# Kernel optimization log

Hardware: AMD Instinct MI355X
Metric: run time of the kernel (lower is better)

Reference implementation:

```python
import jax, jax.numpy as jnp
import numpy as np

EMBED_DIM = 512
NUM_HEADS = 8
HEAD_DIM = EMBED_DIM // NUM_HEADS
LN_EPS = 1e-5


def setup_inputs() -> dict:
    key = jax.random.key(0)
    ks = jax.random.split(key, 7)
    B, S, E = 2, 4096, EMBED_DIM
    s = 1.0 / np.sqrt(E)
    return {
        "x": jax.random.normal(ks[0], (B, S, E), dtype=jnp.float32),
        "qkv_w": jax.random.normal(ks[1], (E, 3 * E), dtype=jnp.float32) * s,
        "qkv_b": jax.random.normal(ks[2], (3 * E,), dtype=jnp.float32) * 0.01,
        "out_w": jax.random.normal(ks[3], (E, E), dtype=jnp.float32) * s,
        "out_b": jax.random.normal(ks[4], (E,), dtype=jnp.float32) * 0.01,
        "ln_g": jnp.ones((E,), dtype=jnp.float32),
        "ln_b": jnp.zeros((E,), dtype=jnp.float32),
    }


def reference(x, qkv_w, qkv_b, out_w, out_b, ln_g, ln_b):
    B, S, E = x.shape
    H, D = NUM_HEADS, HEAD_DIM
    scale = D ** -0.5
    qkv = x @ qkv_w + qkv_b                     # (B, S, 3E)
    qkv = qkv.reshape(B, S, 3, H, D)
    q, k, v = qkv[:, :, 0], qkv[:, :, 1], qkv[:, :, 2]  # (B, S, H, D)
    scores = jnp.einsum("bshd,bthd->bhst", q, k) * scale  # (B, H, S, S)
    probs = jax.nn.softmax(scores, axis=-1)
    ctx = jnp.einsum("bhst,bthd->bshd", probs, v).reshape(B, S, E)
    out = ctx @ out_w + out_b + x               # residual
    mu = out.mean(-1, keepdims=True)
    var = out.var(-1, keepdims=True)
    return (out - mu) * jax.lax.rsqrt(var + LN_EPS) * ln_g + ln_b
```

## Files before the change

kernel.cpp:

```cpp
#include <hip/hip_runtime.h>
#include <stdint.h>

typedef __bf16 bf16x8 __attribute__((ext_vector_type(8)));
typedef float f32x4 __attribute__((ext_vector_type(4)));
typedef float f32x16 __attribute__((ext_vector_type(16)));
typedef float float4v __attribute__((ext_vector_type(4)));
typedef unsigned short u16x4 __attribute__((ext_vector_type(4)));
typedef unsigned short u16x8 __attribute__((ext_vector_type(8)));
typedef unsigned int u32x4v __attribute__((ext_vector_type(4)));

#define DEVI __device__ __forceinline__

static constexpr int Bv = 2, Sv = 4096, Ev = 512, Hv = 8, Dv = 64;
static constexpr int Mv = Bv * Sv;
static constexpr int N3v = 3 * Ev;
static constexpr float QSCALE = 0.125f * 1.4426950408889634f;
static constexpr float C0 = -8.0f;

#if __has_builtin(__builtin_amdgcn_exp2f)
#define EXP2F(x) __builtin_amdgcn_exp2f(x)
#else
#define EXP2F(x) exp2f(x)
#endif

DEVI unsigned short f2bf(float f) {
    unsigned int u = __builtin_bit_cast(unsigned int, f);
    u += 0x7fffu + ((u >> 16) & 1u);
    return (unsigned short)(u >> 16);
}

DEVI float b2f(unsigned short u) {
    return __builtin_bit_cast(float, (unsigned int)u << 16);
}

DEVI unsigned int cvtpk(float lo, float hi) {
    unsigned int r;
    asm("v_cvt_pk_bf16_f32 %0, %1, %2" : "=v"(r) : "v"(lo), "v"(hi));
    return r;
}

DEVI void gload16(const void* src, void* lds) {
    __builtin_amdgcn_global_load_lds(
        (const __attribute__((address_space(1))) unsigned int*)src,
        (__attribute__((address_space(3))) unsigned int*)lds,
        16, 0, 0);
}

__global__ __launch_bounds__(256) void k_prep(const float* __restrict__ x,
                                              unsigned short* __restrict__ xb,
                                              const float* __restrict__ qkv_w,
                                              unsigned short* __restrict__ wqkvT,
                                              const float* __restrict__ out_w,
                                              unsigned short* __restrict__ owT) {
    __shared__ float lds[32][36];
    int blk = blockIdx.x;
    int t = threadIdx.x;
    if (blk < 2048) {
        int n4 = Mv * Ev / 4;
        int i = blk * 256 + t;
        int stride = 2048 * 256;
        for (; i < n4; i += stride) {
            float4v v = ((const float4v*)x)[i];
            u16x4 o;
            o[0] = f2bf(v[0]); o[1] = f2bf(v[1]); o[2] = f2bf(v[2]); o[3] = f2bf(v[3]);
            ((u16x4*)xb)[i] = o;
        }
        return;
    }
    const float* in;
    unsigned short* out;
    int K = 512, N, tile;
    if (blk < 2816) { in = qkv_w; out = wqkvT; N = 1536; tile = blk - 2048; }
    else            { in = out_w; out = owT;   N = 512;  tile = blk - 2816; }
    int tilesN = N >> 5;
    int tn = tile % tilesN, tk = tile / tilesN;
    int k0 = tk << 5, n0 = tn << 5;
    int r = t >> 3, c4 = (t & 7) << 2;
    float4v v = *(const float4v*)(in + (size_t)(k0 + r) * N + n0 + c4);
    *(float4v*)&lds[r][c4] = v;
    __syncthreads();
    int nn = t >> 3, kc = (t & 7) << 2;
    u16x4 o;
#pragma unroll
    for (int j = 0; j < 4; ++j) o[j] = f2bf(lds[kc + j][nn]);
    *(u16x4*)(out + (size_t)(n0 + nn) * K + k0 + kc) = o;
}

template <int EPI>
__global__ __launch_bounds__(256) void k_gemm(
    const unsigned short* __restrict__ A, const unsigned short* __restrict__ Bt,
    int M, int N, int K, const float* __restrict__ bias,
    unsigned short* __restrict__ Qb, unsigned short* __restrict__ Kb,
    unsigned short* __restrict__ Vtb,
    const float* __restrict__ xres, unsigned short* __restrict__ outb) {
    __shared__ char smem[32768];
    char* As = smem;
    char* Bs = smem + 16384;
    int nbt = N >> 7;
    int mb = blockIdx.x / nbt, nbi = blockIdx.x % nbt;
    int m0 = mb << 7, n0 = nbi << 7;
    int tid = threadIdx.x, lane = tid & 63, wave = tid >> 6;
    int wr = wave >> 1, wc = wave & 1;

    f32x4 acc[4][4];
    f32x4 zero = {0.f, 0.f, 0.f, 0.f};
#pragma unroll
    for (int a = 0; a < 4; ++a)
#pragma unroll
        for (int b = 0; b < 4; ++b) acc[a][b] = zero;

    for (int kt = 0; kt < K; kt += 64) {
        __syncthreads();
#pragma unroll
        for (int j = 0; j < 4; ++j) {
            int la = (((wave << 2) + j) << 10) + lane * 16;
            int r = la >> 7, cb = la & 127;
            int cbs = cb ^ ((r & 7) << 4);
            gload16((const char*)(A + (size_t)(m0 + r) * K + kt) + cbs,
                    As + (((wave << 2) + j) << 10));
            gload16((const char*)(Bt + (size_t)(n0 + r) * K + kt) + cbs,
                    Bs + (((wave << 2) + j) << 10));
        }
        asm volatile("s_waitcnt vmcnt(0)" ::: "memory");
        __syncthreads();

        bf16x8 af[4][2], bfr[4][2];
#pragma unroll
        for (int rf = 0; rf < 4; ++rf)
#pragma unroll
            for (int c = 0; c < 2; ++c) {
                int row = (wr << 6) + (rf << 4) + (lane & 15);
                int col = (c << 6) + ((lane >> 4) << 4);
                af[rf][c] = *(const bf16x8*)(As + row * 128 + (col ^ ((row & 7) << 4)));
                int rowb = (wc << 6) + (rf << 4) + (lane & 15);
                bfr[rf][c] = *(const bf16x8*)(Bs + rowb * 128 + (col ^ ((rowb & 7) << 4)));
            }
#pragma unroll
        for (int rf = 0; rf < 4; ++rf)
#pragma unroll
            for (int nf = 0; nf < 4; ++nf)
#pragma unroll
                for (int c = 0; c < 2; ++c)
                    acc[rf][nf] = __builtin_amdgcn_mfma_f32_16x16x32_bf16(
                        af[rf][c], bfr[nf][c], acc[rf][nf], 0, 0, 0);
    }

#pragma unroll
    for (int rf = 0; rf < 4; ++rf)
#pragma unroll
        for (int nf = 0; nf < 4; ++nf) {
            int row0 = m0 + (wr << 6) + (rf << 4) + ((lane >> 4) << 2);
            int col = n0 + (wc << 6) + (nf << 4) + (lane & 15);
            float bv = bias[col];
            if (EPI == 0) {
                int reg = col >> 9, hd = col & 511;
                int h = hd >> 6, d = hd & 63;
                int b = row0 >> 12, s0 = row0 & 4095;
                if (reg == 2) {
                    u16x4 o4;
#pragma unroll
                    for (int i = 0; i < 4; ++i) o4[i] = f2bf(acc[rf][nf][i] + bv);
                    *(u16x4*)(Vtb + ((size_t)((b << 3) + h) * 64 + d) * 4096 + s0) = o4;
                } else {
#pragma unroll
                    for (int i = 0; i < 4; ++i) {
                        float v = acc[rf][nf][i] + bv;
                        size_t idx = ((size_t)((b << 3) + h) * Sv + s0 + i) * Dv + d;
                        if (reg == 0) Qb[idx] = f2bf(v * QSCALE);
                        else          Kb[idx] = f2bf(v);
                    }
                }
            } else {
#pragma unroll
                for (int i = 0; i < 4; ++i) {
                    int row = row0 + i;
                    float v = acc[rf][nf][i] + bv + xres[(size_t)row * N + col];
                    outb[(size_t)row * N + col] = f2bf(v);
                }
            }
        }
}

__global__ __launch_bounds__(256, 2) void k_attn(const unsigned short* __restrict__ Qb,
                                                 const unsigned short* __restrict__ Kb,
                                                 const unsigned short* __restrict__ Vtb,
                                                 unsigned short* __restrict__ po,
                                                 float* __restrict__ pl) {
    __shared__ char smem[24576];
    int bid = blockIdx.x;
    int wg = ((bid & 7) << 6) + (bid >> 3);
    int half = wg & 1, qblk = (wg >> 1) & 15, bh = wg >> 5;
    int tid = threadIdx.x, lane = tid & 63, wave = tid >> 6;
    int l31 = lane & 31, hh = lane >> 5;
    int qbase = (qblk << 8) + (wave << 6);
    int kvbase = half << 11;
    const int NCH = 64;

    const char* Kbase = (const char*)(Kb + (size_t)bh * Sv * Dv + (size_t)kvbase * Dv);
    const char* Vtbase = (const char*)(Vtb + (size_t)bh * Dv * Sv + kvbase);

    bf16x8 qf[2][4];
#pragma unroll
    for (int qs = 0; qs < 2; ++qs)
#pragma unroll
        for (int tp = 0; tp < 4; ++tp)
            qf[qs][tp] = *(const bf16x8*)(Qb + ((size_t)bh * Sv + qbase + (qs << 5) + l31) * Dv +
                                          (tp << 4) + (hh << 3));

    const char* src0;
    const char* src1;
    size_t st0, st1;
    int d0, d1;
    {
        int j0 = wave << 1, j1 = j0 + 1;
        if (j0 < 4) {
            int lo0 = (j0 << 10) + lane * 16, r0 = lo0 >> 7, cb0 = lo0 & 127;
            src0 = Kbase + (size_t)r0 * 128 + (cb0 ^ ((r0 & 7) << 4));
            st0 = 4096; d0 = j0 << 10;
            int lo1 = (j1 << 10) + lane * 16, r1 = lo1 >> 7, cb1 = lo1 & 127;
            src1 = Kbase + (size_t)r1 * 128 + (cb1 ^ ((r1 & 7) << 4));
            st1 = 4096; d1 = j1 << 10;
        } else {
            int lo0 = ((j0 - 4) << 10) + lane * 16, r0 = lo0 >> 6, cb0 = lo0 & 63;
            src0 = Vtbase + (size_t)r0 * 8192 + (cb0 ^ ((r0 & 6) << 3));
            st0 = 64; d0 = 4096 + ((j0 - 4) << 10);
            int lo1 = ((j1 - 4) << 10) + lane * 16, r1 = lo1 >> 6, cb1 = lo1 & 63;
            src1 = Vtbase + (size_t)r1 * 8192 + (cb1 ^ ((r1 & 6) << 3));
            st1 = 64; d1 = 4096 + ((j1 - 4) << 10);
        }
    }

    int koff[4], voff[4];
#pragma unroll
    for (int tp = 0; tp < 4; ++tp)
        koff[tp] = l31 * 128 + (((tp << 5) + (hh << 4)) ^ ((l31 & 7) << 4));
#pragma unroll
    for (int tl = 0; tl < 2; ++tl)
#pragma unroll
        for (int dt = 0; dt < 2; ++dt) {
            int row = (dt << 5) + l31;
            int col = (tl << 5) + (hh << 4);
            voff[tl * 2 + dt] = row * 64 + (col ^ ((row & 6) << 3));
        }

    f32x16 o[2][2];
#pragma unroll
    for (int qs = 0; qs < 2; ++qs)
#pragma unroll
        for (int dt = 0; dt < 2; ++dt)
#pragma unroll
            for (int r = 0; r < 16; ++r) o[qs][dt][r] = 0.f;
    float lsum[2] = {0.f, 0.f};

    gload16(src0, smem + d0);
    gload16(src1, smem + d1);
    gload16(src0 + st0, smem + 8192 + d0);
    gload16(src1 + st1, smem + 8192 + d1);

#define COMPUTE_CHUNK(KSP, VSP)                                                          \
    {                                                                                    \
        bf16x8 kf[4], vf[4];                                                             \
        _Pragma("unroll") for (int tp = 0; tp < 4; ++tp)                                 \
            kf[tp] = *(const bf16x8*)((KSP) + koff[tp]);                                 \
        _Pragma("unroll") for (int i = 0; i < 4; ++i)                                    \
            vf[i] = *(const bf16x8*)((VSP) + voff[i]);                                   \
        _Pragma("unroll") for (int qs = 0; qs < 2; ++qs) {                               \
            f32x16 sc;                                                                   \
            _Pragma("unroll") for (int r = 0; r < 16; ++r) sc[r] = C0;                   \
            __builtin_amdgcn_s_setprio(1);                                               \
            _Pragma("unroll") for (int tp = 0; tp < 4; ++tp)                             \
                sc = __builtin_amdgcn_mfma_f32_32x32x16_bf16(kf[tp], qf[qs][tp], sc, 0, 0, 0); \
            __builtin_amdgcn_s_setprio(0);                                               \
            _Pragma("unroll") for (int r = 0; r < 16; ++r) sc[r] = EXP2F(sc[r]);         \
            float s0 = (sc[0] + sc[1]) + (sc[2] + sc[3]);                                \
            float s1 = (sc[4] + sc[5]) + (sc[6] + sc[7]);                                \
            float s2 = (sc[8] + sc[9]) + (sc[10] + sc[11]);                              \
            float s3 = (sc[12] + sc[13]) + (sc[14] + sc[15]);                            \
            lsum[qs] += (s0 + s1) + (s2 + s3);                                           \
            unsigned int W[8];                                                           \
            _Pragma("unroll") for (int i = 0; i < 8; ++i)                                \
                W[i] = cvtpk(sc[2 * i], sc[2 * i + 1]);                                  \
            _Pragma("unroll") for (int tl = 0; tl < 2; ++tl) {                           \
                unsigned int a1 = W[4 * tl], b1 = W[4 * tl + 2];                         \
                unsigned int a2 = W[4 * tl + 1], b2 = W[4 * tl + 3];                     \
                asm volatile("v_permlane32_swap_b32 %0, %1" : "+v"(a1), "+v"(b1));       \
                asm volatile("v_permlane32_swap_b32 %0, %1" : "+v"(a2), "+v"(b2));       \
                u32x4v uu;                                                               \
                uu[0] = a1; uu[1] = a2; uu[2] = b1; uu[3] = b2;                          \
                bf16x8 pf = __builtin_bit_cast(bf16x8, uu);                              \
                __builtin_amdgcn_s_setprio(1);                                           \
                _Pragma("unroll") for (int dt = 0; dt < 2; ++dt)                         \
                    o[qs][dt] = __builtin_amdgcn_mfma_f32_32x32x16_bf16(                 \
                        vf[tl * 2 + dt], pf, o[qs][dt], 0, 0, 0);                        \
                __builtin_amdgcn_s_setprio(0);                                           \
            }                                                                            \
        }                                                                                \
    }

    int cur = 0;
    for (int kt = 0; kt < NCH - 1; ++kt) {
        asm volatile("s_waitcnt vmcnt(2)\n\ts_barrier" ::: "memory");
        if (kt + 2 < NCH) {
            int tb = cur + 2; if (tb >= 3) tb -= 3;
            gload16(src0 + (size_t)(kt + 2) * st0, smem + tb * 8192 + d0);
            gload16(src1 + (size_t)(kt + 2) * st1, smem + tb * 8192 + d1);
        }
        char* cbuf = smem + cur * 8192;
        COMPUTE_CHUNK(cbuf, cbuf + 4096);
        cur = (cur + 1 == 3) ? 0 : cur + 1;
    }
    asm volatile("s_waitcnt vmcnt(0)\n\ts_barrier" ::: "memory");
    {
        char* cbuf = smem + cur * 8192;
        COMPUTE_CHUNK(cbuf, cbuf + 4096);
    }
#undef COMPUTE_CHUNK

#pragma unroll
    for (int qs = 0; qs < 2; ++qs) {
        float ls = lsum[qs] + __shfl_xor(lsum[qs], 32, 64);
        int qrow = qbase + (qs << 5) + l31;
        if (!hh) pl[((size_t)half * 16 + bh) * Sv + qrow] = ls;
        size_t obase = (((size_t)half * 16 + bh) * Sv + qrow) * 64;
#pragma unroll
        for (int dt = 0; dt < 2; ++dt)
#pragma unroll
            for (int rp = 0; rp < 8; ++rp) {
                int r = rp << 1;
                int d = (dt << 5) + (r & 3) + ((r >> 2) << 3) + (hh << 2);
                unsigned int w = cvtpk(o[qs][dt][r], o[qs][dt][r + 1]);
                *(unsigned int*)(po + obase + d) = w;
            }
    }
}

__global__ __launch_bounds__(256) void k_merge(const unsigned short* __restrict__ po,
                                               const float* __restrict__ pl,
                                               unsigned short* __restrict__ ctx) {
    int t = blockIdx.x * 256 + threadIdx.x;
    int d8 = t & 7, s = (t >> 3) & 4095, bh = t >> 15;
    int b = bh >> 3, h = bh & 7;
    size_t r0 = ((size_t)bh * 4096 + s) * 64 + (d8 << 3);
    size_t r1 = r0 + (size_t)16 * 4096 * 64;
    u16x8 pa = *(const u16x8*)(po + r0);
    u16x8 pb = *(const u16x8*)(po + r1);
    float inv = 1.f / (pl[(size_t)bh * 4096 + s] + pl[(size_t)16 * 4096 + bh * 4096 + s]);
    u32x4v w;
#pragma unroll
    for (int j = 0; j < 4; ++j) {
        float lo = (b2f(pa[2 * j]) + b2f(pb[2 * j])) * inv;
        float hi = (b2f(pa[2 * j + 1]) + b2f(pb[2 * j + 1])) * inv;
        w[j] = cvtpk(lo, hi);
    }
    *(u32x4v*)(ctx + ((size_t)b * 4096 + s) * 512 + (h << 6) + (d8 << 3)) = w;
}

__global__ __launch_bounds__(256) void k_ln(const unsigned short* __restrict__ in,
                                            const float* __restrict__ g,
                                            const float* __restrict__ bta,
                                            float* __restrict__ out) {
    int wave = threadIdx.x >> 6, lane = threadIdx.x & 63;
    size_t row = (size_t)blockIdx.x * 4 + wave;
    u16x8 raw = *(const u16x8*)(in + row * 512 + lane * 8);
    float v[8];
    float s = 0.f, q = 0.f;
#pragma unroll
    for (int j = 0; j < 8; ++j) {
        v[j] = b2f(raw[j]);
        s += v[j];
        q += v[j] * v[j];
    }
#pragma unroll
    for (int off = 1; off < 64; off <<= 1) {
        s += __shfl_xor(s, off, 64);
        q += __shfl_xor(q, off, 64);
    }
    float mu = s * (1.f / 512.f);
    float var = q * (1.f / 512.f) - mu * mu;
    float rs = rsqrtf(var + 1e-5f);
    int c = lane * 8;
    float4v o0, o1;
#pragma unroll
    for (int j = 0; j < 4; ++j) {
        o0[j] = (v[j] - mu) * rs * g[c + j] + bta[c + j];
        o1[j] = (v[4 + j] - mu) * rs * g[c + 4 + j] + bta[c + 4 + j];
    }
    *(float4v*)(out + row * 512 + c) = o0;
    *(float4v*)(out + row * 512 + c + 4) = o1;
}

extern "C" void kernel_launch(void* const* d_in, const int* in_sizes, int n_in,
                              void* d_out, int out_size, void* d_ws, size_t ws_size,
                              hipStream_t stream) {
    const float* x     = (const float*)d_in[0];
    const float* qkv_w = (const float*)d_in[1];
    const float* qkv_b = (const float*)d_in[2];
    const float* out_w = (const float*)d_in[3];
    const float* out_b = (const float*)d_in[4];
    const float* ln_g  = (const float*)d_in[5];
    const float* ln_b  = (const float*)d_in[6];
    float* out = (float*)d_out;
    char* ws = (char*)d_ws;

    unsigned short* owT   = (unsigned short*)(ws);
    unsigned short* wqkvT = (unsigned short*)(ws + 524288);
    unsigned short* Qb    = (unsigned short*)(ws + 2097152);
    unsigned short* Kb    = (unsigned short*)(ws + 10485760);
    unsigned short* Vtb   = (unsigned short*)(ws + 18874368);
    unsigned short* xb    = (unsigned short*)(ws + 27262976);
    unsigned short* po    = (unsigned short*)(ws + 27262976);
    float* pl             = (float*)(ws + 60817408);
    unsigned short* ctxb  = (unsigned short*)(ws + 2097152);
    unsigned short* tmpb  = (unsigned short*)(ws + 10485760);

    k_prep<<<3072, 256, 0, stream>>>(x, xb, qkv_w, wqkvT, out_w, owT);
    k_gemm<0><<<(Mv / 128) * (N3v / 128), 256, 0, stream>>>(
        xb, wqkvT, Mv, N3v, Ev, qkv_b, Qb, Kb, Vtb, nullptr, nullptr);
    k_attn<<<512, 256, 0, stream>>>(Qb, Kb, Vtb, po, pl);
    k_merge<<<2048, 256, 0, stream>>>(po, pl, ctxb);
    k_gemm<1><<<(Mv / 128) * (Ev / 128), 256, 0, stream>>>(
        ctxb, owT, Mv, Ev, Ev, out_b, nullptr, nullptr, nullptr, x, tmpb);
    k_ln<<<Mv / 4, 256, 0, stream>>>(tmpb, ln_g, ln_b, out);
}
```

Baseline: 143.0 us.

## Fuse split-KV merge into attention kernel via last-arriver atomic flag

Removes the separate merge kernel launch. Each attention block now fences its partial output and increments a per-(head, query-block) counter, and the second of the two KV-half blocks to arrive combines both partials and writes the normalized context. This saves a kernel launch and a pass over the partials, and the merge reads data that was just written and may still be in cache. In exchange it adds a memset, atomics and threadfences, and the merge work now runs on only half the attention blocks with a per-thread strided access pattern.

Result: slower. 250.4 us (+75.1%).

```diff
diff --git a/kernel.cpp b/kernel.cpp
--- a/kernel.cpp
+++ b/kernel.cpp
@@ -185,8 +185,11 @@
                                                  const unsigned short* __restrict__ Kb,
                                                  const unsigned short* __restrict__ Vtb,
                                                  unsigned short* __restrict__ po,
-                                                 float* __restrict__ pl) {
+                                                 float* __restrict__ pl,
+                                                 int* __restrict__ flags,
+                                                 unsigned short* __restrict__ ctx) {
     __shared__ char smem[24576];
+    __shared__ int who;
     int bid = blockIdx.x;
     int wg = ((bid & 7) << 6) + (bid >> 3);
     int half = wg & 1, qblk = (wg >> 1) & 15, bh = wg >> 5;
@@ -332,27 +335,33 @@
                 *(unsigned int*)(po + obase + d) = w;
             }
     }
-}
-
-__global__ __launch_bounds__(256) void k_merge(const unsigned short* __restrict__ po,
-                                               const float* __restrict__ pl,
-                                               unsigned short* __restrict__ ctx) {
-    int t = blockIdx.x * 256 + threadIdx.x;
-    int d8 = t & 7, s = (t >> 3) & 4095, bh = t >> 15;
-    int b = bh >> 3, h = bh & 7;
-    size_t r0 = ((size_t)bh * 4096 + s) * 64 + (d8 << 3);
-    size_t r1 = r0 + (size_t)16 * 4096 * 64;
-    u16x8 pa = *(const u16x8*)(po + r0);
-    u16x8 pb = *(const u16x8*)(po + r1);
-    float inv = 1.f / (pl[(size_t)bh * 4096 + s] + pl[(size_t)16 * 4096 + bh * 4096 + s]);
-    u32x4v w;
-#pragma unroll
-    for (int j = 0; j < 4; ++j) {
-        float lo = (b2f(pa[2 * j]) + b2f(pb[2 * j])) * inv;
-        float hi = (b2f(pa[2 * j + 1]) + b2f(pb[2 * j + 1])) * inv;
-        w[j] = cvtpk(lo, hi);
-    }
-    *(u32x4v*)(ctx + ((size_t)b * 4096 + s) * 512 + (h << 6) + (d8 << 3)) = w;
+
+    __threadfence();
+    __syncthreads();
+    if (tid == 0) who = atomicAdd(&flags[(bh << 4) + qblk], 1);
+    __syncthreads();
+    if (who == 1) {
+        __threadfence();
+        int s = (qblk << 8) + tid;
+        size_t r0 = ((size_t)bh * Sv + s) * 64;
+        size_t r1 = r0 + (size_t)16 * Sv * 64;
+        float inv = 1.f / (pl[(size_t)bh * Sv + s] + pl[(size_t)16 * Sv + bh * Sv + s]);
+        int b = bh >> 3, h = bh & 7;
+        size_t cb = ((size_t)b * Sv + s) * Ev + (h << 6);
+#pragma unroll
+        for (int j = 0; j < 8; ++j) {
+            u16x8 pa = *(const u16x8*)(po + r0 + j * 8);
+            u16x8 pb2 = *(const u16x8*)(po + r1 + j * 8);
+            u32x4v w;
+#pragma unroll
+            for (int m = 0; m < 4; ++m) {
+                float lo = (b2f(pa[2 * m]) + b2f(pb2[2 * m])) * inv;
+                float hi = (b2f(pa[2 * m + 1]) + b2f(pb2[2 * m + 1])) * inv;
+                w[m] = cvtpk(lo, hi);
+            }
+            *(u32x4v*)(ctx + cb + j * 8) = w;
+        }
+    }
 }
 
 __global__ __launch_bounds__(256) void k_ln(const unsigned short* __restrict__ in,
@@ -410,14 +419,15 @@
     unsigned short* xb    = (unsigned short*)(ws + 27262976);
     unsigned short* po    = (unsigned short*)(ws + 27262976);
     float* pl             = (float*)(ws + 60817408);
+    int* flags            = (int*)(ws + 61341696);
     unsigned short* ctxb  = (unsigned short*)(ws + 2097152);
     unsigned short* tmpb  = (unsigned short*)(ws + 10485760);
 
+    hipMemsetAsync(flags, 0, 1024, stream);
     k_prep<<<3072, 256, 0, stream>>>(x, xb, qkv_w, wqkvT, out_w, owT);
     k_gemm<0><<<(Mv / 128) * (N3v / 128), 256, 0, stream>>>(
         xb, wqkvT, Mv, N3v, Ev, qkv_b, Qb, Kb, Vtb, nullptr, nullptr);
-    k_attn<<<512, 256, 0, stream>>>(Qb, Kb, Vtb, po, pl);
-    k_merge<<<2048, 256, 0, stream>>>(po, pl, ctxb);
+    k_attn<<<512, 256, 0, stream>>>(Qb, Kb, Vtb, po, pl, flags, ctxb);
     k_gemm<1><<<(Mv / 128) * (Ev / 128), 256, 0, stream>>>(
         ctxb, owT, Mv, Ev, Ev, out_b, nullptr, nullptr, nullptr, x, tmpb);
     k_ln<<<Mv / 4, 256, 0, stream>>>(tmpb, ln_g, ln_b, out);
```
